# Kernel optimization log

Measured on AMD Instinct MI355X. Metric: run time of the kernel, lower is better.

## Reference

```python
import jax, jax.numpy as jnp
import numpy as np

B, S, HIDDEN, H, KVH, D = 4, 1024, 4096, 32, 8, 128
ROT = D // 2  # rotary_dim = head_size/2 (inv_freq over arange(0, dim, 2))
NUM_SLOTS = 8192
ROPE_THETA = 10000.0


def setup_inputs() -> dict:
    key = jax.random.key(0)
    k0, k1, k2 = jax.random.split(key, 3)
    T = B * S
    hidden_states = jax.random.normal(k0, (T, HIDDEN), dtype=jnp.float32) * 0.02
    # RoPE tables: positions 0..S-1 per sequence, gathered per token, shape [T,1,ROT]
    inv_freq = 1.0 / (ROPE_THETA ** (np.arange(0, D, 2, dtype=np.float32) / D))
    pos = jnp.tile(jnp.arange(S, dtype=jnp.float32), B)          # [T]
    freqs = pos[:, None] * jnp.asarray(inv_freq)[None, :]        # [T, ROT]
    cos = jnp.cos(freqs)[:, None, :]
    sin = jnp.sin(freqs)[:, None, :]
    w_qkv = jax.random.normal(k1, (H * D + 2 * KVH * D, HIDDEN), dtype=jnp.float32) * 0.02
    w_o = jax.random.normal(k2, (HIDDEN, H * D), dtype=jnp.float32) * 0.02
    slots = jnp.arange(T, dtype=jnp.int32)
    key_cache = jnp.zeros((NUM_SLOTS, KVH, D), dtype=jnp.float32)
    value_cache = jnp.zeros((NUM_SLOTS, KVH, D), dtype=jnp.float32)
    return {"hidden_states": hidden_states, "cos": cos, "sin": sin,
            "w_qkv": w_qkv, "w_o": w_o,
            "key_cache": key_cache, "value_cache": value_cache,
            "slots": slots, "seq_len": S}


def _rope(x, cos, sin):
    # x: [T, heads, D]; cos/sin: [T, 1, ROT]; NeoX half-split rotation
    x1, x2 = x[..., :ROT], x[..., ROT:2 * ROT]
    return jnp.concatenate([x1 * cos - x2 * sin, x1 * sin + x2 * cos], axis=-1)


def reference(hidden_states, cos, sin, w_qkv, w_o, key_cache, value_cache, slots, seq_len):
    T, hidden = hidden_states.shape
    kvh = key_cache.shape[1]
    d = key_cache.shape[2]
    h = (w_qkv.shape[0] - 2 * kvh * d) // d
    b = T // seq_len
    groups = h // kvh
    scale = d ** -0.5

    # fused QKV projection
    qkv = hidden_states @ w_qkv.T                              # [T, (h+2*kvh)*d]
    q = qkv[:, : h * d].reshape(T, h, d)
    k = qkv[:, h * d: h * d + kvh * d].reshape(T, kvh, d)
    v = qkv[:, h * d + kvh * d:].reshape(T, kvh, d)

    # in-place RoPE on query and key
    q = _rope(q, cos, sin)
    k = _rope(k, cos, sin)

    # reshape_and_cache: scatter rotated K and V into slot-indexed cache
    new_key_cache = key_cache.at[slots].set(k)
    new_value_cache = value_cache.at[slots].set(v)

    # prefill varlen flash attention (equal-length sequences), causal, GQA
    qb = q.reshape(b, seq_len, h, d)
    kb = jnp.repeat(k.reshape(b, seq_len, kvh, d), groups, axis=2)  # [b,s,h,d]
    vb = jnp.repeat(v.reshape(b, seq_len, kvh, d), groups, axis=2)
    scores = jnp.einsum('bqhd,bkhd->bhqk', qb, kb) * scale
    causal = jnp.tril(jnp.ones((seq_len, seq_len), dtype=bool))
    scores = jnp.where(causal[None, None], scores, jnp.finfo(scores.dtype).min)
    attn = jax.nn.softmax(scores, axis=-1)
    out = jnp.einsum('bhqk,bkhd->bqhd', attn, vb).reshape(T, h * d)

    return out @ w_o.T, new_key_cache, new_value_cache
```

## Files before the change

### kernel.cpp

```cpp
#include <hip/hip_runtime.h>
#include <hip/hip_bf16.h>

#define B_    4
#define S_    1024
#define HID   4096
#define H_    32
#define KVH_  8
#define D_    128
#define T_    (B_ * S_)
#define QKVD  (H_ * D_ + 2 * KVH_ * D_)
#define NSLOT 8192

typedef __attribute__((ext_vector_type(8))) short short8;
typedef __attribute__((ext_vector_type(4))) float f32x4;

__device__ __forceinline__ unsigned short f2b(float f) {
  union { __hip_bfloat16 h; unsigned short u; } c;
  c.h = __float2bfloat16(f);
  return c.u;
}

__device__ __forceinline__ void async16(const void* g, void* l) {
  __builtin_amdgcn_global_load_lds(
      (const __attribute__((address_space(1))) unsigned int*)g,
      (__attribute__((address_space(3))) unsigned int*)l,
      16, 0, 0);
}

__global__ void conv_bf16(const float* __restrict__ src,
                          unsigned short* __restrict__ dst, int n4) {
  int i = blockIdx.x * 256 + threadIdx.x;
  if (i >= n4) return;
  float4 v = reinterpret_cast<const float4*>(src)[i];
  ushort4 o;
  o.x = f2b(v.x); o.y = f2b(v.y); o.z = f2b(v.z); o.w = f2b(v.w);
  reinterpret_cast<ushort4*>(dst)[i] = o;
}

__global__ __launch_bounds__(256) void gemm_bt(
    const unsigned short* __restrict__ A, const unsigned short* __restrict__ Bm,
    float* __restrict__ C, int M, int N, int K) {
  __shared__ unsigned short As[128 * 32];
  __shared__ unsigned short Bs[128 * 32];
  const int tid  = threadIdx.x;
  const int lane = tid & 63;
  const int w    = tid >> 6;
  const int quad = lane >> 4;
  const int l16  = lane & 15;
  const int bm = blockIdx.y * 128;
  const int bn = blockIdx.x * 128;
  const int wm = (w >> 1) * 64;
  const int wn = (w & 1) * 64;

  const int srow = tid >> 2;
  const int scol = (tid & 3) * 8;
  const size_t a0 = (size_t)(bm + srow) * K + scol;
  const size_t a1 = (size_t)(bm + 64 + srow) * K + scol;
  const size_t b0 = (size_t)(bn + srow) * K + scol;
  const size_t b1 = (size_t)(bn + 64 + srow) * K + scol;

  f32x4 acc[4][4];
#pragma unroll
  for (int i = 0; i < 4; i++)
#pragma unroll
    for (int j = 0; j < 4; j++)
#pragma unroll
      for (int r = 0; r < 4; r++) acc[i][j][r] = 0.f;

  for (int k0 = 0; k0 < K; k0 += 32) {
    async16(A + a0 + k0, As + tid * 8);
    async16(A + a1 + k0, As + 2048 + tid * 8);
    async16(Bm + b0 + k0, Bs + tid * 8);
    async16(Bm + b1 + k0, Bs + 2048 + tid * 8);
    __syncthreads();
    short8 a[4], b[4];
#pragma unroll
    for (int i = 0; i < 4; i++)
      a[i] = *(const short8*)(As + (wm + i * 16 + l16) * 32 + quad * 8);
#pragma unroll
    for (int j = 0; j < 4; j++)
      b[j] = *(const short8*)(Bs + (wn + j * 16 + l16) * 32 + quad * 8);
#pragma unroll
    for (int i = 0; i < 4; i++)
#pragma unroll
      for (int j = 0; j < 4; j++)
        acc[i][j] = __builtin_amdgcn_mfma_f32_16x16x32_bf16(a[i], b[j], acc[i][j], 0, 0, 0);
    __syncthreads();
  }
  const int crow0 = bm + wm + quad * 4;
  const int ccol0 = bn + wn + l16;
#pragma unroll
  for (int i = 0; i < 4; i++)
#pragma unroll
    for (int j = 0; j < 4; j++)
#pragma unroll
      for (int r = 0; r < 4; r++)
        C[(size_t)(crow0 + i * 16 + r) * N + ccol0 + j * 16] = acc[i][j][r];
}

__global__ void rope_scatter(
    const float* __restrict__ qkv, const float* __restrict__ cosb,
    const float* __restrict__ sinb, const int* __restrict__ slots,
    unsigned short* __restrict__ qb, unsigned short* __restrict__ kb,
    unsigned short* __restrict__ vb, float* __restrict__ kco,
    float* __restrict__ vco) {
  const int t = blockIdx.x;
  const int tid = threadIdx.x;
  const int b = t >> 10, s = t & 1023;
  const float* row = qkv + (size_t)t * QKVD;
  const float* cs = cosb + (size_t)t * 64;
  const float* sn = sinb + (size_t)t * 64;
  const int slot = slots[t];
  for (int wk = tid; wk < H_ * 64; wk += 256) {
    int hh = wk >> 6, i = wk & 63;
    float x1 = row[hh * D_ + i], x2 = row[hh * D_ + 64 + i];
    float c = cs[i], sv = sn[i];
    size_t base = ((size_t)(b * H_ + hh) * S_ + s) * D_;
    qb[base + i]      = f2b(x1 * c - x2 * sv);
    qb[base + 64 + i] = f2b(x1 * sv + x2 * c);
  }
  for (int wk = tid; wk < KVH_ * 64; wk += 256) {
    int hh = wk >> 6, i = wk & 63;
    float x1 = row[H_ * D_ + hh * D_ + i], x2 = row[H_ * D_ + hh * D_ + 64 + i];
    float c = cs[i], sv = sn[i];
    float o1 = x1 * c - x2 * sv, o2 = x1 * sv + x2 * c;
    size_t base = ((size_t)(b * KVH_ + hh) * S_ + s) * D_;
    kb[base + i] = f2b(o1);
    kb[base + 64 + i] = f2b(o2);
    size_t cb = ((size_t)slot * KVH_ + hh) * D_;
    kco[cb + i] = o1;
    kco[cb + 64 + i] = o2;
  }
  for (int wk = tid; wk < KVH_ * D_; wk += 256) {
    int hh = wk >> 7, i = wk & 127;
    float x = row[H_ * D_ + KVH_ * D_ + hh * D_ + i];
    vb[((size_t)(b * KVH_ + hh) * S_ + s) * D_ + i] = f2b(x);
    vco[((size_t)slot * KVH_ + hh) * D_ + i] = x;
  }
}

__global__ void transpose_v(const unsigned short* __restrict__ vb,
                            unsigned short* __restrict__ vt) {
  __shared__ unsigned short tile[64][65];
  const int bid = blockIdx.x;
  const int dt = bid & 1, st = (bid >> 1) & 15, bk = bid >> 5;
  const int tid = threadIdx.x;
  const unsigned short* src = vb + ((size_t)bk * S_ + st * 64) * D_ + dt * 64;
#pragma unroll
  for (int k = 0; k < 16; k++) {
    int e = k * 256 + tid, r = e >> 6, c = e & 63;
    tile[r][c] = src[(size_t)r * D_ + c];
  }
  __syncthreads();
  unsigned short* dst = vt + ((size_t)bk * D_ + dt * 64) * S_ + st * 64;
#pragma unroll
  for (int k = 0; k < 16; k++) {
    int e = k * 256 + tid, r = e >> 6, c = e & 63;
    dst[(size_t)r * S_ + c] = tile[c][r];
  }
}

__global__ __launch_bounds__(256) void attn_fused(
    const unsigned short* __restrict__ qb, const unsigned short* __restrict__ kb,
    const unsigned short* __restrict__ vt, unsigned short* __restrict__ ob) {
  __shared__ unsigned short Ks[4 * 64 * 32];
  __shared__ unsigned short Vs[2 * 128 * 32];
  __shared__ unsigned short Ps[4][2 * 16 * 32];
  const int tid = threadIdx.x;
  const int lane = tid & 63, w = tid >> 6;
  const int quad = lane >> 4, l16 = lane & 15;
  const int bidx = blockIdx.x;
  const int qt = 15 - (bidx & 15);
  const int bh = bidx >> 4;
  const int h = bh & 31, b = bh >> 5;
  const int kvh = h >> 2;
  const int q0 = qt * 64;
  const unsigned short* qbase = qb + ((size_t)bh * S_ + q0) * D_;
  const unsigned short* kbase = kb + (size_t)(b * KVH_ + kvh) * S_ * D_;
  const unsigned short* vbase = vt + (size_t)(b * KVH_ + kvh) * D_ * S_;

  const int srow = tid >> 2;
  const int scol = (tid & 3) * 8;

#pragma unroll
  for (int i = 0; i < 4; i++)
    async16(qbase + (size_t)srow * D_ + i * 32 + scol, (unsigned short*)Ks + i * 2048 + tid * 8);
  __syncthreads();
  short8 qf[4];
#pragma unroll
  for (int kc = 0; kc < 4; kc++)
    qf[kc] = *(const short8*)(Ks + (kc * 64 + w * 16 + l16) * 32 + quad * 8);

  f32x4 oac[8];
#pragma unroll
  for (int n = 0; n < 8; n++)
#pragma unroll
    for (int r = 0; r < 4; r++) oac[n][r] = 0.f;
  float m_run[4] = {-3.0e38f, -3.0e38f, -3.0e38f, -3.0e38f};
  float l_run[4] = {0.f, 0.f, 0.f, 0.f};
  const float sl2 = 0.08838834764831843f * 1.4426950408889634f;

  for (int jt = 0; jt <= qt; jt++) {
    __syncthreads();
    const int j0 = jt * 64;
#pragma unroll
    for (int i = 0; i < 4; i++)
      async16(kbase + (size_t)(j0 + srow) * D_ + i * 32 + scol,
              (unsigned short*)Ks + i * 2048 + tid * 8);
#pragma unroll
    for (int i = 0; i < 4; i++) {
      int kc = i >> 1;
      int d = (i & 1) * 64 + srow;
      async16(vbase + (size_t)d * S_ + j0 + kc * 32 + scol,
              (unsigned short*)Vs + i * 2048 + tid * 8);
    }
    __syncthreads();

    f32x4 sac[4];
#pragma unroll
    for (int t = 0; t < 4; t++)
#pragma unroll
      for (int r = 0; r < 4; r++) sac[t][r] = 0.f;
#pragma unroll
    for (int t = 0; t < 4; t++)
#pragma unroll
      for (int kc = 0; kc < 4; kc++)
        sac[t] = __builtin_amdgcn_mfma_f32_16x16x32_bf16(
            qf[kc], *(const short8*)(Ks + (kc * 64 + t * 16 + l16) * 32 + quad * 8),
            sac[t], 0, 0, 0);

    const int qrow = q0 + w * 16 + quad * 4;
#pragma unroll
    for (int t = 0; t < 4; t++) {
      const int kcol = j0 + t * 16 + l16;
#pragma unroll
      for (int r = 0; r < 4; r++) {
        float v = sac[t][r] * sl2;
        if (jt == qt && kcol > qrow + r) v = -3.0e38f;
        sac[t][r] = v;
      }
    }
    float mx[4];
#pragma unroll
    for (int r = 0; r < 4; r++)
      mx[r] = fmaxf(fmaxf(sac[0][r], sac[1][r]), fmaxf(sac[2][r], sac[3][r]));
#pragma unroll
    for (int off = 1; off < 16; off <<= 1)
#pragma unroll
      for (int r = 0; r < 4; r++) mx[r] = fmaxf(mx[r], __shfl_xor(mx[r], off));
    float alpha[4];
#pragma unroll
    for (int r = 0; r < 4; r++) {
      float mn = fmaxf(m_run[r], mx[r]);
      alpha[r] = exp2f(m_run[r] - mn);
      m_run[r] = mn;
    }
    float rs[4] = {0.f, 0.f, 0.f, 0.f};
    unsigned short* psw = &Ps[w][0];
#pragma unroll
    for (int t = 0; t < 4; t++)
#pragma unroll
      for (int r = 0; r < 4; r++) {
        float p = exp2f(sac[t][r] - m_run[r]);
        rs[r] += p;
        psw[((t >> 1) * 16 + quad * 4 + r) * 32 + (t & 1) * 16 + l16] = f2b(p);
      }
#pragma unroll
    for (int off = 1; off < 16; off <<= 1)
#pragma unroll
      for (int r = 0; r < 4; r++) rs[r] += __shfl_xor(rs[r], off);
#pragma unroll
    for (int r = 0; r < 4; r++) l_run[r] = l_run[r] * alpha[r] + rs[r];
#pragma unroll
    for (int n = 0; n < 8; n++)
#pragma unroll
      for (int r = 0; r < 4; r++) oac[n][r] *= alpha[r];
#pragma unroll
    for (int kc = 0; kc < 2; kc++) {
      short8 pf = *(const short8*)(psw + (kc * 16 + l16) * 32 + quad * 8);
#pragma unroll
      for (int n = 0; n < 8; n++)
        oac[n] = __builtin_amdgcn_mfma_f32_16x16x32_bf16(
            pf, *(const short8*)(Vs + (kc * 128 + n * 16 + l16) * 32 + quad * 8),
            oac[n], 0, 0, 0);
    }
  }
  float inv[4];
#pragma unroll
  for (int r = 0; r < 4; r++) inv[r] = 1.0f / l_run[r];
  const size_t trow = (size_t)(b * S_ + q0 + w * 16 + quad * 4);
#pragma unroll
  for (int n = 0; n < 8; n++)
#pragma unroll
    for (int r = 0; r < 4; r++)
      ob[(trow + r) * (size_t)(H_ * D_) + h * D_ + n * 16 + l16] =
          f2b(oac[n][r] * inv[r]);
}

extern "C" void kernel_launch(void* const* d_in, const int* in_sizes, int n_in,
                              void* d_out, int out_size, void* d_ws, size_t ws_size,
                              hipStream_t stream) {
  const float* hidden = (const float*)d_in[0];
  const float* cosb   = (const float*)d_in[1];
  const float* sinb   = (const float*)d_in[2];
  const float* wqkv   = (const float*)d_in[3];
  const float* wo     = (const float*)d_in[4];
  const float* kc_in  = (const float*)d_in[5];
  const float* vc_in  = (const float*)d_in[6];
  const int*   slots  = (const int*)d_in[7];

  float* out    = (float*)d_out;
  float* kc_out = out + (size_t)T_ * HID;
  float* vc_out = kc_out + (size_t)NSLOT * KVH_ * D_;

  char* ws = (char*)d_ws;
  unsigned short* hb    = (unsigned short*)ws; ws += (size_t)T_ * HID * 2;
  unsigned short* wqkvb = (unsigned short*)ws; ws += (size_t)QKVD * HID * 2;
  unsigned short* wob   = (unsigned short*)ws; ws += (size_t)HID * HID * 2;
  float*          qkv   = (float*)ws;          ws += (size_t)T_ * QKVD * 4;
  unsigned short* qb    = (unsigned short*)ws; ws += (size_t)T_ * H_ * D_ * 2;
  unsigned short* kb    = (unsigned short*)ws; ws += (size_t)T_ * KVH_ * D_ * 2;
  unsigned short* vb    = (unsigned short*)ws; ws += (size_t)T_ * KVH_ * D_ * 2;
  unsigned short* vt    = (unsigned short*)ws; ws += (size_t)T_ * KVH_ * D_ * 2;
  unsigned short* ob    = (unsigned short*)ws;

  const size_t cache_bytes = (size_t)NSLOT * KVH_ * D_ * 4;
  hipMemcpyAsync(kc_out, kc_in, cache_bytes, hipMemcpyDeviceToDevice, stream);
  hipMemcpyAsync(vc_out, vc_in, cache_bytes, hipMemcpyDeviceToDevice, stream);

  conv_bf16<<<(T_ * HID / 4) / 256, 256, 0, stream>>>(hidden, hb, T_ * HID / 4);
  conv_bf16<<<(QKVD * HID / 4) / 256, 256, 0, stream>>>(wqkv, wqkvb, QKVD * HID / 4);
  conv_bf16<<<(HID * HID / 4) / 256, 256, 0, stream>>>(wo, wob, HID * HID / 4);

  dim3 g1(QKVD / 128, T_ / 128);
  gemm_bt<<<g1, 256, 0, stream>>>(hb, wqkvb, qkv, T_, QKVD, HID);

  rope_scatter<<<T_, 256, 0, stream>>>(qkv, cosb, sinb, slots, qb, kb, vb, kc_out, vc_out);

  transpose_v<<<B_ * KVH_ * 16 * 2, 256, 0, stream>>>(vb, vt);

  attn_fused<<<B_ * H_ * (S_ / 64), 256, 0, stream>>>(qb, kb, vt, ob);

  dim3 g2(HID / 128, T_ / 128);
  gemm_bt<<<g2, 256, 0, stream>>>(ob, wob, out, T_, HID, HID);
}
```

Baseline: 1.032 ms.

## Swizzle LDS layouts, group GEMM tiles, prescale Q, and compute row sums via MFMA

Adds an XOR swizzle to the LDS tile layouts in both the GEMM and the attention kernel so that MFMA fragment reads hit fewer bank conflicts. It also remaps GEMM block indices into column groups for better L2 reuse. In attention, the softmax scale is folded into Q during RoPE, the causal mask is applied only on the diagonal tile, and the row sums come from an extra MFMA against a ones vector instead of shuffle reductions. The risks are the added bf16 rounding of the prescaled Q, and that the swizzle has to match exactly between the async loads and the fragment reads.

```diff
diff --git a/kernel.cpp b/kernel.cpp
--- a/kernel.cpp
+++ b/kernel.cpp
@@ -47,13 +47,21 @@
   const int w    = tid >> 6;
   const int quad = lane >> 4;
   const int l16  = lane & 15;
-  const int bm = blockIdx.y * 128;
-  const int bn = blockIdx.x * 128;
+
+  {
+  }
+  const int p = blockIdx.x + gridDim.x * blockIdx.y;
+  const int tpg = 8 * gridDim.y;
+  const int g = p / tpg, rr = p % tpg;
+  const int bm = (rr >> 3) * 128;
+  const int bn = (g * 8 + (rr & 7)) * 128;
+
   const int wm = (w >> 1) * 64;
   const int wn = (w & 1) * 64;
 
   const int srow = tid >> 2;
-  const int scol = (tid & 3) * 8;
+  const int scol = (((tid & 3) ^ ((tid >> 3) & 3)) * 8);
+  const int qoff = (quad ^ ((l16 >> 1) & 3)) * 8;
   const size_t a0 = (size_t)(bm + srow) * K + scol;
   const size_t a1 = (size_t)(bm + 64 + srow) * K + scol;
   const size_t b0 = (size_t)(bn + srow) * K + scol;
@@ -76,10 +84,10 @@
     short8 a[4], b[4];
 #pragma unroll
     for (int i = 0; i < 4; i++)
-      a[i] = *(const short8*)(As + (wm + i * 16 + l16) * 32 + quad * 8);
+      a[i] = *(const short8*)(As + (wm + i * 16 + l16) * 32 + qoff);
 #pragma unroll
     for (int j = 0; j < 4; j++)
-      b[j] = *(const short8*)(Bs + (wn + j * 16 + l16) * 32 + quad * 8);
+      b[j] = *(const short8*)(Bs + (wn + j * 16 + l16) * 32 + qoff);
 #pragma unroll
     for (int i = 0; i < 4; i++)
 #pragma unroll
@@ -104,6 +112,7 @@
     unsigned short* __restrict__ qb, unsigned short* __restrict__ kb,
     unsigned short* __restrict__ vb, float* __restrict__ kco,
     float* __restrict__ vco) {
+  const float sl2 = 0.08838834764831843f * 1.4426950408889634f;
   const int t = blockIdx.x;
   const int tid = threadIdx.x;
   const int b = t >> 10, s = t & 1023;
@@ -116,8 +125,8 @@
     float x1 = row[hh * D_ + i], x2 = row[hh * D_ + 64 + i];
     float c = cs[i], sv = sn[i];
     size_t base = ((size_t)(b * H_ + hh) * S_ + s) * D_;
-    qb[base + i]      = f2b(x1 * c - x2 * sv);
-    qb[base + 64 + i] = f2b(x1 * sv + x2 * c);
+    qb[base + i]      = f2b((x1 * c - x2 * sv) * sl2);
+    qb[base + 64 + i] = f2b((x1 * sv + x2 * c) * sl2);
   }
   for (int wk = tid; wk < KVH_ * 64; wk += 256) {
     int hh = wk >> 6, i = wk & 63;
@@ -180,7 +189,8 @@
   const unsigned short* vbase = vt + (size_t)(b * KVH_ + kvh) * D_ * S_;
 
   const int srow = tid >> 2;
-  const int scol = (tid & 3) * 8;
+  const int scol = (((tid & 3) ^ ((tid >> 3) & 3)) * 8);
+  const int qoff = (quad ^ ((l16 >> 1) & 3)) * 8;
 
 #pragma unroll
   for (int i = 0; i < 4; i++)
@@ -189,18 +199,29 @@
   short8 qf[4];
 #pragma unroll
   for (int kc = 0; kc < 4; kc++)
-    qf[kc] = *(const short8*)(Ks + (kc * 64 + w * 16 + l16) * 32 + quad * 8);
+    qf[kc] = *(const short8*)(Ks + (kc * 64 + w * 16 + l16) * 32 + qoff);
+
+  short8 of;
+  {
+    unsigned short ov = (l16 == 0) ? (unsigned short)0x3F80 : (unsigned short)0;
+#pragma unroll
+    for (int j = 0; j < 8; j++) of[j] = (short)ov;
+  }
 
   f32x4 oac[8];
+  f32x4 osum;
 #pragma unroll
   for (int n = 0; n < 8; n++)
 #pragma unroll
     for (int r = 0; r < 4; r++) oac[n][r] = 0.f;
+#pragma unroll
+  for (int r = 0; r < 4; r++) osum[r] = 0.f;
   float m_run[4] = {-3.0e38f, -3.0e38f, -3.0e38f, -3.0e38f};
-  float l_run[4] = {0.f, 0.f, 0.f, 0.f};
-  const float sl2 = 0.08838834764831843f * 1.4426950408889634f;
-
-  for (int jt = 0; jt <= qt; jt++) {
+
+  unsigned short* psw = &Ps[w][0];
+  const int qrow = q0 + w * 16 + quad * 4;
+
+  auto body = [&](int jt, bool domask) {
     __syncthreads();
     const int j0 = jt * 64;
 #pragma unroll
@@ -226,18 +247,16 @@
 #pragma unroll
       for (int kc = 0; kc < 4; kc++)
         sac[t] = __builtin_amdgcn_mfma_f32_16x16x32_bf16(
-            qf[kc], *(const short8*)(Ks + (kc * 64 + t * 16 + l16) * 32 + quad * 8),
+            qf[kc], *(const short8*)(Ks + (kc * 64 + t * 16 + l16) * 32 + qoff),
             sac[t], 0, 0, 0);
 
-    const int qrow = q0 + w * 16 + quad * 4;
-#pragma unroll
-    for (int t = 0; t < 4; t++) {
-      const int kcol = j0 + t * 16 + l16;
-#pragma unroll
-      for (int r = 0; r < 4; r++) {
-        float v = sac[t][r] * sl2;
-        if (jt == qt && kcol > qrow + r) v = -3.0e38f;
-        sac[t][r] = v;
+    if (domask) {
+#pragma unroll
+      for (int t = 0; t < 4; t++) {
+        const int kcol = j0 + t * 16 + l16;
+#pragma unroll
+        for (int r = 0; r < 4; r++)
+          if (kcol > qrow + r) sac[t][r] = -3.0e38f;
       }
     }
     float mx[4];
@@ -255,39 +274,42 @@
       alpha[r] = exp2f(m_run[r] - mn);
       m_run[r] = mn;
     }
-    float rs[4] = {0.f, 0.f, 0.f, 0.f};
-    unsigned short* psw = &Ps[w][0];
 #pragma unroll
     for (int t = 0; t < 4; t++)
 #pragma unroll
       for (int r = 0; r < 4; r++) {
         float p = exp2f(sac[t][r] - m_run[r]);
-        rs[r] += p;
-        psw[((t >> 1) * 16 + quad * 4 + r) * 32 + (t & 1) * 16 + l16] = f2b(p);
+        int prow = quad * 4 + r;
+        int chunk = (((t & 1) * 2 + (l16 >> 3)) ^ ((prow >> 1) & 3));
+        psw[(t >> 1) * 512 + prow * 32 + chunk * 8 + (l16 & 7)] = f2b(p);
       }
 #pragma unroll
-    for (int off = 1; off < 16; off <<= 1)
-#pragma unroll
-      for (int r = 0; r < 4; r++) rs[r] += __shfl_xor(rs[r], off);
-#pragma unroll
-    for (int r = 0; r < 4; r++) l_run[r] = l_run[r] * alpha[r] + rs[r];
+    for (int r = 0; r < 4; r++) osum[r] *= alpha[r];
 #pragma unroll
     for (int n = 0; n < 8; n++)
 #pragma unroll
       for (int r = 0; r < 4; r++) oac[n][r] *= alpha[r];
 #pragma unroll
     for (int kc = 0; kc < 2; kc++) {
-      short8 pf = *(const short8*)(psw + (kc * 16 + l16) * 32 + quad * 8);
+      short8 pf = *(const short8*)(psw + kc * 512 + l16 * 32 + qoff);
+      osum = __builtin_amdgcn_mfma_f32_16x16x32_bf16(pf, of, osum, 0, 0, 0);
 #pragma unroll
       for (int n = 0; n < 8; n++)
         oac[n] = __builtin_amdgcn_mfma_f32_16x16x32_bf16(
-            pf, *(const short8*)(Vs + (kc * 128 + n * 16 + l16) * 32 + quad * 8),
+            pf, *(const short8*)(Vs + (kc * 128 + n * 16 + l16) * 32 + qoff),
             oac[n], 0, 0, 0);
     }
-  }
+  };
+
+  for (int jt = 0; jt < qt; jt++) body(jt, false);
+  body(qt, true);
+
   float inv[4];
 #pragma unroll
-  for (int r = 0; r < 4; r++) inv[r] = 1.0f / l_run[r];
+  for (int r = 0; r < 4; r++) {
+    float l = __shfl(osum[r], lane & 48, 64);
+    inv[r] = 1.0f / l;
+  }
   const size_t trow = (size_t)(b * S_ + q0 + w * 16 + quad * 4);
 #pragma unroll
   for (int n = 0; n < 8; n++)
```

Measured after the change: 1.175 ms. 1.14x slower.
